# Kernel tuning notes

Measured on AMD Instinct MI355X. Metric: run time of the kernel, lower is better.

The kernel has to match this reference:

```python
import jax, jax.numpy as jnp
import numpy as np

N = 40000
E = 640000
DIN = 128
H = 128
G = 16
C = 10


def setup_inputs() -> dict:
    key = jax.random.key(0)
    ks = jax.random.split(key, 12)
    x = jax.random.normal(ks[0], (N, DIN), dtype=jnp.float32)
    edge_index = jax.random.randint(ks[1], (2, E), 0, N, dtype=jnp.int64)
    batch = jnp.sort(jax.random.randint(ks[2], (N,), 0, G, dtype=jnp.int64))
    s = 1.0 / np.sqrt(H)
    W_in = jax.random.normal(ks[3], (DIN, H), dtype=jnp.float32) * s
    b_in = jnp.zeros((H,), dtype=jnp.float32)
    W1 = jax.random.normal(ks[4], (H, H), dtype=jnp.float32) * s
    b1 = jnp.zeros((H,), dtype=jnp.float32)
    W2 = jax.random.normal(ks[5], (H, H), dtype=jnp.float32) * s
    b2 = jnp.zeros((H,), dtype=jnp.float32)
    Wf1 = jax.random.normal(ks[6], (H, H // 2), dtype=jnp.float32) * s
    bf1 = jnp.zeros((H // 2,), dtype=jnp.float32)
    Wf2 = jax.random.normal(ks[7], (H // 2, C), dtype=jnp.float32) * (1.0 / np.sqrt(H // 2))
    bf2 = jnp.zeros((C,), dtype=jnp.float32)
    return {"x": x, "edge_index": edge_index, "batch": batch,
            "W_in": W_in, "b_in": b_in, "W1": W1, "b1": b1,
            "W2": W2, "b2": b2, "Wf1": Wf1, "bf1": bf1,
            "Wf2": Wf2, "bf2": bf2}


def _gcn_conv(h, src, dst, deg_inv_sqrt, W, b):
    # h' = D^{-1/2} (A + I) D^{-1/2} (h W) + b  (PyG GCNConv with self-loops)
    hw = h @ W  # [N, H]
    norm = deg_inv_sqrt[src] * deg_inv_sqrt[dst]  # [E]
    agg = jax.ops.segment_sum(hw[src] * norm[:, None], dst, num_segments=N)
    agg = agg + hw * (deg_inv_sqrt * deg_inv_sqrt)[:, None]  # self-loop term
    return agg + b


def reference(x, edge_index, batch, W_in, b_in, W1, b1, W2, b2, Wf1, bf1, Wf2, bf2):
    src, dst = edge_index[0], edge_index[1]
    # degree on target nodes, including self-loop (+1)
    deg = jax.ops.segment_sum(jnp.ones((E,), dtype=x.dtype), dst, num_segments=N) + 1.0
    deg_inv_sqrt = jax.lax.rsqrt(deg)

    h = x @ W_in + b_in
    h = jax.nn.relu(_gcn_conv(h, src, dst, deg_inv_sqrt, W1, b1))  # dropout is identity in eval
    h = jax.nn.relu(_gcn_conv(h, src, dst, deg_inv_sqrt, W2, b2))

    # global mean pool by graph id
    sums = jax.ops.segment_sum(h, batch, num_segments=G)  # [G, H]
    counts = jax.ops.segment_sum(jnp.ones((N,), dtype=h.dtype), batch, num_segments=G)
    pooled = sums / jnp.maximum(counts, 1.0)[:, None]

    out = jax.nn.relu(pooled @ Wf1 + bf1) @ Wf2 + bf2  # [G, C]
    return out
```

## Files before the change

kernel.cpp:

```cpp
#include <hip/hip_runtime.h>

#define NN 40000
#define EE 640000
#define NCH 157

typedef unsigned int uint;
typedef unsigned short ushort;
typedef __attribute__((ext_vector_type(8))) short short8;
typedef __attribute__((ext_vector_type(4))) float floatx4;

__device__ inline ushort f2bf(float f) {
    uint u = __float_as_uint(f);
    return (ushort)((u + 0x7fffu + ((u >> 16) & 1u)) >> 16);
}
__device__ inline float bf_lo(uint u) { return __uint_as_float(u << 16); }
__device__ inline float bf_hi(uint u) { return __uint_as_float(u & 0xffff0000u); }

__device__ inline int lower_bound_dev(const int* __restrict__ a, int n, int x) {
    int lo = 0, hi = n;
    while (lo < hi) { int m = (lo + hi) >> 1; if (a[m] < x) lo = m + 1; else hi = m; }
    return lo;
}

__global__ __launch_bounds__(256) void histprep_kernel(const int* __restrict__ dst,
                                                       int* __restrict__ counts,
                                                       const float* __restrict__ W_in,
                                                       const float* __restrict__ W1,
                                                       const float* __restrict__ b_in,
                                                       const float* __restrict__ W2,
                                                       const int* __restrict__ batch,
                                                       ushort* __restrict__ Bp1,
                                                       ushort* __restrict__ Bp2,
                                                       float* __restrict__ cvec,
                                                       int* __restrict__ glo) {
    int b = blockIdx.x, t = threadIdx.x;
    if (b < 2500) {
        atomicAdd(&counts[dst[b * 256 + t]], 1);
    } else if (b < 2564) {
        int idx = (b - 2500) * 256 + t;
        int k = idx >> 7, n = idx & 127;
        float s = 0.f;
        for (int j = 0; j < 128; ++j) s = fmaf(W_in[k * 128 + j], W1[j * 128 + n], s);
        Bp1[((size_t)(k >> 3) * 128 + n) * 8 + (k & 7)] = f2bf(s);
    } else if (b < 2628) {
        int idx = (b - 2564) * 256 + t;
        int k = idx >> 7, n = idx & 127;
        Bp2[((size_t)(k >> 3) * 128 + n) * 8 + (k & 7)] = f2bf(W2[idx]);
    } else {
        if (t < 128) {
            float s = 0.f;
            for (int k = 0; k < 128; ++k) s = fmaf(b_in[k], W1[k * 128 + t], s);
            cvec[t] = s;
        } else if (t < 128 + 17) {
            int g = t - 128;
            glo[g] = lower_bound_dev(batch, NN, g);
        }
    }
}

__global__ __launch_bounds__(256) void scan_kernel(const int* __restrict__ counts,
                                                   int* __restrict__ goff,
                                                   int* __restrict__ start,
                                                   int* __restrict__ cursor,
                                                   float* __restrict__ dis, int N) {
    __shared__ int ws[4];
    __shared__ int sbase;
    int t = threadIdx.x, lane = t & 63, wv = t >> 6;
    int idx = blockIdx.x * 256 + t;
    int c = (idx < N) ? counts[idx] : 0;
    int v = c;
    #pragma unroll
    for (int d = 1; d < 64; d <<= 1) {
        int u = __shfl_up(v, d, 64);
        if (lane >= d) v += u;
    }
    if (lane == 63) ws[wv] = v;
    __syncthreads();
    if (t == 0) {
        int total = ws[0] + ws[1] + ws[2] + ws[3];
        sbase = atomicAdd(goff, total);
    }
    __syncthreads();
    int off = sbase;
    for (int j = 0; j < wv; ++j) off += ws[j];
    if (idx < N) {
        int excl = off + v - c;
        start[idx] = excl;
        cursor[idx] = excl;
        dis[idx] = rsqrtf((float)c + 1.0f);
    }
}

template <bool ABF16>
__device__ inline void mm_tile(const void* __restrict__ Av, const ushort* __restrict__ Bpack,
                               ushort* __restrict__ C, int tile, int wv, int lane) {
    int m = lane & 15, q = lane >> 4;
    int row = tile * 64 + wv * 16 + m;

    short8 afr[4];
    if (ABF16) {
        const ushort* A = (const ushort*)Av;
        const ushort* ap = A + (size_t)row * 128 + q * 8;
        #pragma unroll
        for (int k0 = 0; k0 < 4; ++k0) afr[k0] = *(const short8*)(ap + k0 * 32);
    } else {
        const float* A = (const float*)Av;
        const float* ap = A + (size_t)row * 128 + q * 8;
        #pragma unroll
        for (int k0 = 0; k0 < 4; ++k0) {
            float4 f0 = *(const float4*)(ap + k0 * 32);
            float4 f1 = *(const float4*)(ap + k0 * 32 + 4);
            short8 a;
            a[0] = (short)f2bf(f0.x); a[1] = (short)f2bf(f0.y);
            a[2] = (short)f2bf(f0.z); a[3] = (short)f2bf(f0.w);
            a[4] = (short)f2bf(f1.x); a[5] = (short)f2bf(f1.y);
            a[6] = (short)f2bf(f1.z); a[7] = (short)f2bf(f1.w);
            afr[k0] = a;
        }
    }

    floatx4 acc[8];
    #pragma unroll
    for (int nt = 0; nt < 8; ++nt) { floatx4 z = {0.f, 0.f, 0.f, 0.f}; acc[nt] = z; }

    #pragma unroll
    for (int nt = 0; nt < 8; ++nt) {
        #pragma unroll
        for (int k0 = 0; k0 < 4; ++k0) {
            short8 bfrag = *(const short8*)(Bpack + ((size_t)(k0 * 4 + q) * 128 + nt * 16 + m) * 8);
            acc[nt] = __builtin_amdgcn_mfma_f32_16x16x32_bf16(afr[k0], bfrag, acc[nt], 0, 0, 0);
        }
    }

    int orow_base = tile * 64 + wv * 16 + q * 4;
    #pragma unroll
    for (int nt = 0; nt < 8; ++nt) {
        #pragma unroll
        for (int r = 0; r < 4; ++r)
            C[(size_t)(orow_base + r) * 128 + nt * 16 + m] = f2bf(acc[nt][r]);
    }
}

__global__ __launch_bounds__(256) void fillmm1_kernel(const int* __restrict__ src,
                                                      const int* __restrict__ dst,
                                                      const float* __restrict__ dis,
                                                      int* __restrict__ cursor,
                                                      int2* __restrict__ edata,
                                                      const float* __restrict__ x,
                                                      const ushort* __restrict__ Bp1,
                                                      ushort* __restrict__ bufA) {
    int b = blockIdx.x, t = threadIdx.x;
    if (b < 2500) {
        int e = b * 256 + t;
        int s = src[e], d = dst[e];
        int pos = atomicAdd(&cursor[d], 1);
        float nrm = dis[s] * dis[d];
        int2 v; v.x = s; v.y = __float_as_int(nrm);
        edata[pos] = v;
    } else {
        mm_tile<false>(x, Bp1, bufA, b - 2500, t >> 6, t & 63);
    }
}

__global__ __launch_bounds__(256) void mm2_kernel(const ushort* __restrict__ A,
                                                  const ushort* __restrict__ Bp2,
                                                  ushort* __restrict__ C) {
    mm_tile<true>(A, Bp2, C, blockIdx.x, threadIdx.x >> 6, threadIdx.x & 63);
}

__global__ __launch_bounds__(256) void agg_kernel(const ushort* __restrict__ hw,
                                                  const float* __restrict__ dis,
                                                  const int* __restrict__ start,
                                                  const int* __restrict__ counts,
                                                  const int2* __restrict__ edata,
                                                  const float* __restrict__ cvec,
                                                  const float* __restrict__ bias,
                                                  ushort* __restrict__ out, int N) {
    __shared__ int2 eds[4][64];
    int wv = threadIdx.x >> 6;
    int lane = threadIdx.x & 63;
    int i = blockIdx.x * 4 + wv;
    if (i >= N) return;
    int beg = start[i];
    int deg = counts[i];
    int dmain = deg > 64 ? 64 : deg;
    const uint* __restrict__ hv = (const uint*)hw;

    int2 ed;
    if (lane < dmain) ed = edata[beg + lane];
    else { ed.x = i; ed.y = 0; }
    eds[wv][lane] = ed;

    float di = dis[i];
    float sii = di * di;
    uint su = hv[(size_t)i * 64 + lane];
    float a0 = sii * bf_lo(su);
    float a1 = sii * bf_hi(su);
    float sumnorm = sii;

    int dpad = (dmain + 7) & ~7;
    for (int j = 0; j < dpad; j += 8) {
        int2 e0 = eds[wv][j],     e1 = eds[wv][j + 1];
        int2 e2 = eds[wv][j + 2], e3 = eds[wv][j + 3];
        int2 e4 = eds[wv][j + 4], e5 = eds[wv][j + 5];
        int2 e6 = eds[wv][j + 6], e7 = eds[wv][j + 7];
        uint u0 = hv[(size_t)e0.x * 64 + lane];
        uint u1 = hv[(size_t)e1.x * 64 + lane];
        uint u2 = hv[(size_t)e2.x * 64 + lane];
        uint u3 = hv[(size_t)e3.x * 64 + lane];
        uint u4 = hv[(size_t)e4.x * 64 + lane];
        uint u5 = hv[(size_t)e5.x * 64 + lane];
        uint u6 = hv[(size_t)e6.x * 64 + lane];
        uint u7 = hv[(size_t)e7.x * 64 + lane];
        float n0 = __int_as_float(e0.y), n1 = __int_as_float(e1.y);
        float n2 = __int_as_float(e2.y), n3 = __int_as_float(e3.y);
        float n4 = __int_as_float(e4.y), n5 = __int_as_float(e5.y);
        float n6 = __int_as_float(e6.y), n7 = __int_as_float(e7.y);
        a0 = fmaf(n0, bf_lo(u0), a0); a1 = fmaf(n0, bf_hi(u0), a1);
        a0 = fmaf(n1, bf_lo(u1), a0); a1 = fmaf(n1, bf_hi(u1), a1);
        a0 = fmaf(n2, bf_lo(u2), a0); a1 = fmaf(n2, bf_hi(u2), a1);
        a0 = fmaf(n3, bf_lo(u3), a0); a1 = fmaf(n3, bf_hi(u3), a1);
        a0 = fmaf(n4, bf_lo(u4), a0); a1 = fmaf(n4, bf_hi(u4), a1);
        a0 = fmaf(n5, bf_lo(u5), a0); a1 = fmaf(n5, bf_hi(u5), a1);
        a0 = fmaf(n6, bf_lo(u6), a0); a1 = fmaf(n6, bf_hi(u6), a1);
        a0 = fmaf(n7, bf_lo(u7), a0); a1 = fmaf(n7, bf_hi(u7), a1);
        sumnorm += ((n0 + n1) + (n2 + n3)) + ((n4 + n5) + (n6 + n7));
    }
    for (int e = beg + 64; e < beg + deg; ++e) {
        int2 et = edata[e];
        float n0 = __int_as_float(et.y);
        uint u0 = hv[(size_t)et.x * 64 + lane];
        a0 = fmaf(n0, bf_lo(u0), a0);
        a1 = fmaf(n0, bf_hi(u0), a1);
        sumnorm += n0;
    }

    float c0 = 0.f, c1 = 0.f;
    if (cvec) { c0 = cvec[2 * lane]; c1 = cvec[2 * lane + 1]; }
    float b0 = bias[2 * lane], b1 = bias[2 * lane + 1];
    float o0 = fmaxf(fmaf(sumnorm, c0, a0) + b0, 0.f);
    float o1 = fmaxf(fmaf(sumnorm, c1, a1) + b1, 0.f);
    uint o = (uint)f2bf(o0) | ((uint)f2bf(o1) << 16);
    ((uint*)out)[(size_t)i * 64 + lane] = o;
}

__global__ __launch_bounds__(256) void poolfinal_kernel(const ushort* __restrict__ h,
                                                        const int* __restrict__ glo,
                                                        float* __restrict__ pools,
                                                        int* __restrict__ ticket,
                                                        const float* __restrict__ Wf1,
                                                        const float* __restrict__ bf1,
                                                        const float* __restrict__ Wf2,
                                                        const float* __restrict__ bf2,
                                                        float* __restrict__ out) {
    __shared__ float pooled[16][128];
    __shared__ float z[16][64];
    __shared__ int slast;
    int t = threadIdx.x, c2 = t & 63, wv = t >> 6;
    int b = blockIdx.x;
    int g = b >> 3, ch = b & 7;
    int lo = glo[g], hi = glo[g + 1];
    int span = hi - lo;
    int chunk = (span + 7) >> 3;
    int r0 = lo + ch * chunk;
    int r1 = hi < r0 + chunk ? hi : r0 + chunk;
    const uint* __restrict__ hv = (const uint*)h;

    float a0 = 0.f, a1 = 0.f;
    #pragma unroll 4
    for (int j = r0 + wv; j < r1; j += 4) {
        uint u = hv[(size_t)j * 64 + c2];
        a0 += bf_lo(u);
        a1 += bf_hi(u);
    }
    if (r0 < r1) {
        atomicAdd(&pools[g * 128 + 2 * c2], a0);
        atomicAdd(&pools[g * 128 + 2 * c2 + 1], a1);
    }

    __syncthreads();
    __threadfence();
    if (t == 0) slast = atomicAdd(ticket, 1);
    __syncthreads();
    if (slast != 127) return;

    for (int idx = t; idx < 2048; idx += 256) {
        int gg = idx >> 7, c = idx & 127;
        int cn = glo[gg + 1] - glo[gg];
        float cnf = (float)(cn > 1 ? cn : 1);
        float ps = __hip_atomic_load(&pools[idx], __ATOMIC_RELAXED, __HIP_MEMORY_SCOPE_AGENT);
        pooled[gg][c] = ps / cnf;
    }
    __syncthreads();
    for (int idx = t; idx < 1024; idx += 256) {
        int gg = idx >> 6, j = idx & 63;
        float s = bf1[j];
        for (int k = 0; k < 128; ++k) s = fmaf(pooled[gg][k], Wf1[k * 64 + j], s);
        z[gg][j] = fmaxf(s, 0.f);
    }
    __syncthreads();
    if (t < 160) {
        int gg = t / 10, k = t % 10;
        float s = bf2[k];
        for (int j = 0; j < 64; ++j) s = fmaf(z[gg][j], Wf2[j * 10 + k], s);
        out[t] = s;
    }
}


extern "C" void kernel_launch(void* const* d_in, const int* in_sizes, int n_in,
                              void* d_out, int out_size, void* d_ws, size_t ws_size,
                              hipStream_t stream) {
    const float* x    = (const float*)d_in[0];
    const int* edge   = (const int*)d_in[1];
    const int* batch  = (const int*)d_in[2];
    const float* W_in = (const float*)d_in[3];
    const float* b_in = (const float*)d_in[4];
    const float* W1   = (const float*)d_in[5];
    const float* b1   = (const float*)d_in[6];
    const float* W2   = (const float*)d_in[7];
    const float* b2   = (const float*)d_in[8];
    const float* Wf1  = (const float*)d_in[9];
    const float* bf1  = (const float*)d_in[10];
    const float* Wf2  = (const float*)d_in[11];
    const float* bf2  = (const float*)d_in[12];
    float* out = (float*)d_out;

    char* ws = (char*)d_ws;
    size_t off = 0;
    auto alloc = [&](size_t bytes) -> void* {
        void* p = ws + off;
        off += (bytes + 511) & ~(size_t)511;
        return p;
    };
    int* counts   = (int*)alloc((size_t)NN * 4);
    float* pools  = (float*)alloc(16 * 128 * 4);
    int* misc     = (int*)alloc(512);
    size_t zero_bytes = off;
    int* goff     = misc;
    int* ticket   = misc + 1;
    int* glo      = misc + 8;
    ushort* bufA  = (ushort*)alloc((size_t)NN * 128 * 2);
    ushort* bufB  = (ushort*)alloc((size_t)NN * 128 * 2);
    ushort* Bp1   = (ushort*)alloc(128 * 128 * 2);
    ushort* Bp2   = (ushort*)alloc(128 * 128 * 2);
    float* cvec   = (float*)alloc(128 * 4);
    float* dis    = (float*)alloc((size_t)NN * 4);
    int* start    = (int*)alloc((size_t)NN * 4);
    int* cursor   = (int*)alloc((size_t)NN * 4);
    int2* edata   = (int2*)alloc((size_t)EE * 8);

    hipMemsetAsync(counts, 0, zero_bytes, stream);

    histprep_kernel<<<2629, 256, 0, stream>>>(edge + EE, counts, W_in, W1, b_in, W2,
                                              batch, Bp1, Bp2, cvec, glo);
    scan_kernel<<<NCH, 256, 0, stream>>>(counts, goff, start, cursor, dis, NN);
    fillmm1_kernel<<<2500 + NN / 64, 256, 0, stream>>>(edge, edge + EE, dis, cursor,
                                                       edata, x, Bp1, bufA);
    agg_kernel<<<NN / 4, 256, 0, stream>>>(bufA, dis, start, counts, edata, cvec, b1, bufB, NN);
    mm2_kernel<<<NN / 64, 256, 0, stream>>>(bufB, Bp2, bufA);
    agg_kernel<<<NN / 4, 256, 0, stream>>>(bufA, dis, start, counts, edata, nullptr, b2, bufB, NN);
    poolfinal_kernel<<<128, 256, 0, stream>>>(bufB, glo, pools, ticket,
                                              Wf1, bf1, Wf2, bf2, out);
}
```

Before: 243.1 us.

## Gather neighbor rows with 16-byte loads, four edges per wave in parallel

The aggregation kernel now has each 16-lane quarter of a wave load a full 256-byte bf16 neighbor row as uint4, so four edges are gathered at once instead of one row per wave with 4-byte loads. Each lane keeps eight partial accumulators, and the quarters are combined with cross-lane shuffles before bias, ReLU and a single vectorized store. The goal is fewer, wider memory instructions and more independent gathers in flight. In exchange it uses more registers, adds a shuffle reduction, pads the edge list to multiples of 16, and leaves the overflow tail for nodes with more than 64 edges running on only one quarter of the wave.

```diff
diff --git a/kernel.cpp b/kernel.cpp
--- a/kernel.cpp
+++ b/kernel.cpp
@@ -179,69 +179,111 @@
     __shared__ int2 eds[4][64];
     int wv = threadIdx.x >> 6;
     int lane = threadIdx.x & 63;
+    int q = lane & 15, h4 = lane >> 4;
     int i = blockIdx.x * 4 + wv;
     if (i >= N) return;
     int beg = start[i];
     int deg = counts[i];
     int dmain = deg > 64 ? 64 : deg;
-    const uint* __restrict__ hv = (const uint*)hw;
+    const uint4* __restrict__ hv4 = (const uint4*)hw;
 
     int2 ed;
     if (lane < dmain) ed = edata[beg + lane];
     else { ed.x = i; ed.y = 0; }
     eds[wv][lane] = ed;
 
+    float a0 = 0.f, a1 = 0.f, a2 = 0.f, a3 = 0.f;
+    float a4 = 0.f, a5 = 0.f, a6 = 0.f, a7 = 0.f;
+    float sumnorm = 0.f;
+
+    int dpad = (dmain + 15) & ~15;
+    for (int j = 0; j < dpad; j += 16) {
+        int2 e0 = eds[wv][j + h4];
+        int2 e1 = eds[wv][j + 4 + h4];
+        int2 e2 = eds[wv][j + 8 + h4];
+        int2 e3 = eds[wv][j + 12 + h4];
+        uint4 u0 = hv4[(size_t)e0.x * 16 + q];
+        uint4 u1 = hv4[(size_t)e1.x * 16 + q];
+        uint4 u2 = hv4[(size_t)e2.x * 16 + q];
+        uint4 u3 = hv4[(size_t)e3.x * 16 + q];
+        float n0 = __int_as_float(e0.y), n1 = __int_as_float(e1.y);
+        float n2 = __int_as_float(e2.y), n3 = __int_as_float(e3.y);
+        a0 = fmaf(n0, bf_lo(u0.x), a0); a1 = fmaf(n0, bf_hi(u0.x), a1);
+        a2 = fmaf(n0, bf_lo(u0.y), a2); a3 = fmaf(n0, bf_hi(u0.y), a3);
+        a4 = fmaf(n0, bf_lo(u0.z), a4); a5 = fmaf(n0, bf_hi(u0.z), a5);
+        a6 = fmaf(n0, bf_lo(u0.w), a6); a7 = fmaf(n0, bf_hi(u0.w), a7);
+        a0 = fmaf(n1, bf_lo(u1.x), a0); a1 = fmaf(n1, bf_hi(u1.x), a1);
+        a2 = fmaf(n1, bf_lo(u1.y), a2); a3 = fmaf(n1, bf_hi(u1.y), a3);
+        a4 = fmaf(n1, bf_lo(u1.z), a4); a5 = fmaf(n1, bf_hi(u1.z), a5);
+        a6 = fmaf(n1, bf_lo(u1.w), a6); a7 = fmaf(n1, bf_hi(u1.w), a7);
+        a0 = fmaf(n2, bf_lo(u2.x), a0); a1 = fmaf(n2, bf_hi(u2.x), a1);
+        a2 = fmaf(n2, bf_lo(u2.y), a2); a3 = fmaf(n2, bf_hi(u2.y), a3);
+        a4 = fmaf(n2, bf_lo(u2.z), a4); a5 = fmaf(n2, bf_hi(u2.z), a5);
+        a6 = fmaf(n2, bf_lo(u2.w), a6); a7 = fmaf(n2, bf_hi(u2.w), a7);
+        a0 = fmaf(n3, bf_lo(u3.x), a0); a1 = fmaf(n3, bf_hi(u3.x), a1);
+        a2 = fmaf(n3, bf_lo(u3.y), a2); a3 = fmaf(n3, bf_hi(u3.y), a3);
+        a4 = fmaf(n3, bf_lo(u3.z), a4); a5 = fmaf(n3, bf_hi(u3.z), a5);
+        a6 = fmaf(n3, bf_lo(u3.w), a6); a7 = fmaf(n3, bf_hi(u3.w), a7);
+        sumnorm += (n0 + n1) + (n2 + n3);
+    }
+    for (int e = beg + 64; e < beg + deg; ++e) {
+        int2 et = edata[e];
+        if (h4 == 0) {
+            float n0 = __int_as_float(et.y);
+            uint4 u = hv4[(size_t)et.x * 16 + q];
+            a0 = fmaf(n0, bf_lo(u.x), a0); a1 = fmaf(n0, bf_hi(u.x), a1);
+            a2 = fmaf(n0, bf_lo(u.y), a2); a3 = fmaf(n0, bf_hi(u.y), a3);
+            a4 = fmaf(n0, bf_lo(u.z), a4); a5 = fmaf(n0, bf_hi(u.z), a5);
+            a6 = fmaf(n0, bf_lo(u.w), a6); a7 = fmaf(n0, bf_hi(u.w), a7);
+            sumnorm += n0;
+        }
+    }
+
+    a0 += __shfl_xor(a0, 16); a0 += __shfl_xor(a0, 32);
+    a1 += __shfl_xor(a1, 16); a1 += __shfl_xor(a1, 32);
+    a2 += __shfl_xor(a2, 16); a2 += __shfl_xor(a2, 32);
+    a3 += __shfl_xor(a3, 16); a3 += __shfl_xor(a3, 32);
+    a4 += __shfl_xor(a4, 16); a4 += __shfl_xor(a4, 32);
+    a5 += __shfl_xor(a5, 16); a5 += __shfl_xor(a5, 32);
+    a6 += __shfl_xor(a6, 16); a6 += __shfl_xor(a6, 32);
+    a7 += __shfl_xor(a7, 16); a7 += __shfl_xor(a7, 32);
+    sumnorm += __shfl_xor(sumnorm, 16); sumnorm += __shfl_xor(sumnorm, 32);
+
     float di = dis[i];
     float sii = di * di;
-    uint su = hv[(size_t)i * 64 + lane];
-    float a0 = sii * bf_lo(su);
-    float a1 = sii * bf_hi(su);
-    float sumnorm = sii;
-
-    int dpad = (dmain + 7) & ~7;
-    for (int j = 0; j < dpad; j += 8) {
-        int2 e0 = eds[wv][j],     e1 = eds[wv][j + 1];
-        int2 e2 = eds[wv][j + 2], e3 = eds[wv][j + 3];
-        int2 e4 = eds[wv][j + 4], e5 = eds[wv][j + 5];
-        int2 e6 = eds[wv][j + 6], e7 = eds[wv][j + 7];
-        uint u0 = hv[(size_t)e0.x * 64 + lane];
-        uint u1 = hv[(size_t)e1.x * 64 + lane];
-        uint u2 = hv[(size_t)e2.x * 64 + lane];
-        uint u3 = hv[(size_t)e3.x * 64 + lane];
-        uint u4 = hv[(size_t)e4.x * 64 + lane];
-        uint u5 = hv[(size_t)e5.x * 64 + lane];
-        uint u6 = hv[(size_t)e6.x * 64 + lane];
-        uint u7 = hv[(size_t)e7.x * 64 + lane];
-        float n0 = __int_as_float(e0.y), n1 = __int_as_float(e1.y);
-        float n2 = __int_as_float(e2.y), n3 = __int_as_float(e3.y);
-        float n4 = __int_as_float(e4.y), n5 = __int_as_float(e5.y);
-        float n6 = __int_as_float(e6.y), n7 = __int_as_float(e7.y);
-        a0 = fmaf(n0, bf_lo(u0), a0); a1 = fmaf(n0, bf_hi(u0), a1);
-        a0 = fmaf(n1, bf_lo(u1), a0); a1 = fmaf(n1, bf_hi(u1), a1);
-        a0 = fmaf(n2, bf_lo(u2), a0); a1 = fmaf(n2, bf_hi(u2), a1);
-        a0 = fmaf(n3, bf_lo(u3), a0); a1 = fmaf(n3, bf_hi(u3), a1);
-        a0 = fmaf(n4, bf_lo(u4), a0); a1 = fmaf(n4, bf_hi(u4), a1);
-        a0 = fmaf(n5, bf_lo(u5), a0); a1 = fmaf(n5, bf_hi(u5), a1);
-        a0 = fmaf(n6, bf_lo(u6), a0); a1 = fmaf(n6, bf_hi(u6), a1);
-        a0 = fmaf(n7, bf_lo(u7), a0); a1 = fmaf(n7, bf_hi(u7), a1);
-        sumnorm += ((n0 + n1) + (n2 + n3)) + ((n4 + n5) + (n6 + n7));
-    }
-    for (int e = beg + 64; e < beg + deg; ++e) {
-        int2 et = edata[e];
-        float n0 = __int_as_float(et.y);
-        uint u0 = hv[(size_t)et.x * 64 + lane];
-        a0 = fmaf(n0, bf_lo(u0), a0);
-        a1 = fmaf(n0, bf_hi(u0), a1);
-        sumnorm += n0;
-    }
-
-    float c0 = 0.f, c1 = 0.f;
-    if (cvec) { c0 = cvec[2 * lane]; c1 = cvec[2 * lane + 1]; }
-    float b0 = bias[2 * lane], b1 = bias[2 * lane + 1];
-    float o0 = fmaxf(fmaf(sumnorm, c0, a0) + b0, 0.f);
-    float o1 = fmaxf(fmaf(sumnorm, c1, a1) + b1, 0.f);
-    uint o = (uint)f2bf(o0) | ((uint)f2bf(o1) << 16);
-    ((uint*)out)[(size_t)i * 64 + lane] = o;
+    uint4 su = hv4[(size_t)i * 16 + q];
+    a0 = fmaf(sii, bf_lo(su.x), a0); a1 = fmaf(sii, bf_hi(su.x), a1);
+    a2 = fmaf(sii, bf_lo(su.y), a2); a3 = fmaf(sii, bf_hi(su.y), a3);
+    a4 = fmaf(sii, bf_lo(su.z), a4); a5 = fmaf(sii, bf_hi(su.z), a5);
+    a6 = fmaf(sii, bf_lo(su.w), a6); a7 = fmaf(sii, bf_hi(su.w), a7);
+    sumnorm += sii;
+
+    float c0 = 0.f, c1 = 0.f, c2 = 0.f, c3 = 0.f;
+    float c4 = 0.f, c5 = 0.f, c6 = 0.f, c7 = 0.f;
+    if (cvec) {
+        float4 ca = *(const float4*)(cvec + 8 * q);
+        float4 cb = *(const float4*)(cvec + 8 * q + 4);
+        c0 = ca.x; c1 = ca.y; c2 = ca.z; c3 = ca.w;
+        c4 = cb.x; c5 = cb.y; c6 = cb.z; c7 = cb.w;
+    }
+    float4 ba = *(const float4*)(bias + 8 * q);
+    float4 bb = *(const float4*)(bias + 8 * q + 4);
+    float o0 = fmaxf(fmaf(sumnorm, c0, a0) + ba.x, 0.f);
+    float o1 = fmaxf(fmaf(sumnorm, c1, a1) + ba.y, 0.f);
+    float o2 = fmaxf(fmaf(sumnorm, c2, a2) + ba.z, 0.f);
+    float o3 = fmaxf(fmaf(sumnorm, c3, a3) + ba.w, 0.f);
+    float o4 = fmaxf(fmaf(sumnorm, c4, a4) + bb.x, 0.f);
+    float o5 = fmaxf(fmaf(sumnorm, c5, a5) + bb.y, 0.f);
+    float o6 = fmaxf(fmaf(sumnorm, c6, a6) + bb.z, 0.f);
+    float o7 = fmaxf(fmaf(sumnorm, c7, a7) + bb.w, 0.f);
+    if (h4 == 0) {
+        uint4 o;
+        o.x = (uint)f2bf(o0) | ((uint)f2bf(o1) << 16);
+        o.y = (uint)f2bf(o2) | ((uint)f2bf(o3) << 16);
+        o.z = (uint)f2bf(o4) | ((uint)f2bf(o5) << 16);
+        o.w = (uint)f2bf(o6) | ((uint)f2bf(o7) << 16);
+        ((uint4*)out)[(size_t)i * 16 + q] = o;
+    }
 }
 
 __global__ __launch_bounds__(256) void poolfinal_kernel(const ushort* __restrict__ h,
```

Result: no change. 241.4 us (-0.7%).

## Split hw into column-quarter planes and aggregate per quarter for cache locality

Applied to the files above, without the earlier changes.

The matmul now writes its bf16 output as four column-quarter planes of 32 features each, and aggregation runs four times as many blocks. Each block handles one quarter, with 16 lanes per edge row and 4 edges gathered in parallel, followed by a shuffle reduction. The aim is a smaller per-pass gather working set that fits in cache, plus nontemporal loads and stores for streamed data. The cost is re-reading the edge list four times and extra shuffle and launch overhead.

```diff
diff --git a/kernel.cpp b/kernel.cpp
--- a/kernel.cpp
+++ b/kernel.cpp
@@ -3,6 +3,7 @@
 #define NN 40000
 #define EE 640000
 #define NCH 157
+#define NQB (NN / 4)
 
 typedef unsigned int uint;
 typedef unsigned short ushort;
@@ -135,9 +136,10 @@
     int orow_base = tile * 64 + wv * 16 + q * 4;
     #pragma unroll
     for (int nt = 0; nt < 8; ++nt) {
+        size_t cbase = (size_t)(nt >> 1) * ((size_t)NN * 32) + (size_t)((nt & 1) * 16 + m);
         #pragma unroll
         for (int r = 0; r < 4; ++r)
-            C[(size_t)(orow_base + r) * 128 + nt * 16 + m] = f2bf(acc[nt][r]);
+            C[cbase + (size_t)(orow_base + r) * 32] = f2bf(acc[nt][r]);
     }
 }
 
@@ -168,80 +170,91 @@
     mm_tile<true>(A, Bp2, C, blockIdx.x, threadIdx.x >> 6, threadIdx.x & 63);
 }
 
-__global__ __launch_bounds__(256) void agg_kernel(const ushort* __restrict__ hw,
-                                                  const float* __restrict__ dis,
-                                                  const int* __restrict__ start,
-                                                  const int* __restrict__ counts,
-                                                  const int2* __restrict__ edata,
-                                                  const float* __restrict__ cvec,
-                                                  const float* __restrict__ bias,
-                                                  ushort* __restrict__ out, int N) {
+__global__ __launch_bounds__(256) void aggq_kernel(const ushort* __restrict__ hw,
+                                                   const float* __restrict__ dis,
+                                                   const int* __restrict__ start,
+                                                   const int* __restrict__ counts,
+                                                   const int2* __restrict__ edata,
+                                                   const float* __restrict__ cvec,
+                                                   const float* __restrict__ bias,
+                                                   ushort* __restrict__ out, int N) {
     __shared__ int2 eds[4][64];
     int wv = threadIdx.x >> 6;
     int lane = threadIdx.x & 63;
-    int i = blockIdx.x * 4 + wv;
+    int qb = blockIdx.x / NQB;
+    int b  = blockIdx.x - qb * NQB;
+    int i = b * 4 + wv;
     if (i >= N) return;
+    int m16 = lane & 15, h4 = lane >> 4;
     int beg = start[i];
     int deg = counts[i];
     int dmain = deg > 64 ? 64 : deg;
-    const uint* __restrict__ hv = (const uint*)hw;
+    const uint* __restrict__ hvq = (const uint*)(hw + (size_t)qb * NN * 32);
 
     int2 ed;
-    if (lane < dmain) ed = edata[beg + lane];
-    else { ed.x = i; ed.y = 0; }
+    if (lane < dmain) {
+        long long e64 = __builtin_nontemporal_load((const long long*)(edata + beg + lane));
+        ed.x = (int)(unsigned long long)e64;
+        ed.y = (int)((unsigned long long)e64 >> 32);
+    } else {
+        ed.x = i; ed.y = 0;
+    }
     eds[wv][lane] = ed;
 
-    float di = dis[i];
-    float sii = di * di;
-    uint su = hv[(size_t)i * 64 + lane];
-    float a0 = sii * bf_lo(su);
-    float a1 = sii * bf_hi(su);
-    float sumnorm = sii;
-
-    int dpad = (dmain + 7) & ~7;
-    for (int j = 0; j < dpad; j += 8) {
-        int2 e0 = eds[wv][j],     e1 = eds[wv][j + 1];
-        int2 e2 = eds[wv][j + 2], e3 = eds[wv][j + 3];
-        int2 e4 = eds[wv][j + 4], e5 = eds[wv][j + 5];
-        int2 e6 = eds[wv][j + 6], e7 = eds[wv][j + 7];
-        uint u0 = hv[(size_t)e0.x * 64 + lane];
-        uint u1 = hv[(size_t)e1.x * 64 + lane];
-        uint u2 = hv[(size_t)e2.x * 64 + lane];
-        uint u3 = hv[(size_t)e3.x * 64 + lane];
-        uint u4 = hv[(size_t)e4.x * 64 + lane];
-        uint u5 = hv[(size_t)e5.x * 64 + lane];
-        uint u6 = hv[(size_t)e6.x * 64 + lane];
-        uint u7 = hv[(size_t)e7.x * 64 + lane];
+    float a0 = 0.f, a1 = 0.f, sn = 0.f;
+
+    int dpad = (dmain + 15) & ~15;
+    for (int j = 0; j < dpad; j += 16) {
+        int2 e0 = eds[wv][j + h4];
+        int2 e1 = eds[wv][j + 4 + h4];
+        int2 e2 = eds[wv][j + 8 + h4];
+        int2 e3 = eds[wv][j + 12 + h4];
+        uint u0 = hvq[(size_t)e0.x * 16 + m16];
+        uint u1 = hvq[(size_t)e1.x * 16 + m16];
+        uint u2 = hvq[(size_t)e2.x * 16 + m16];
+        uint u3 = hvq[(size_t)e3.x * 16 + m16];
         float n0 = __int_as_float(e0.y), n1 = __int_as_float(e1.y);
         float n2 = __int_as_float(e2.y), n3 = __int_as_float(e3.y);
-        float n4 = __int_as_float(e4.y), n5 = __int_as_float(e5.y);
-        float n6 = __int_as_float(e6.y), n7 = __int_as_float(e7.y);
         a0 = fmaf(n0, bf_lo(u0), a0); a1 = fmaf(n0, bf_hi(u0), a1);
         a0 = fmaf(n1, bf_lo(u1), a0); a1 = fmaf(n1, bf_hi(u1), a1);
         a0 = fmaf(n2, bf_lo(u2), a0); a1 = fmaf(n2, bf_hi(u2), a1);
         a0 = fmaf(n3, bf_lo(u3), a0); a1 = fmaf(n3, bf_hi(u3), a1);
-        a0 = fmaf(n4, bf_lo(u4), a0); a1 = fmaf(n4, bf_hi(u4), a1);
-        a0 = fmaf(n5, bf_lo(u5), a0); a1 = fmaf(n5, bf_hi(u5), a1);
-        a0 = fmaf(n6, bf_lo(u6), a0); a1 = fmaf(n6, bf_hi(u6), a1);
-        a0 = fmaf(n7, bf_lo(u7), a0); a1 = fmaf(n7, bf_hi(u7), a1);
-        sumnorm += ((n0 + n1) + (n2 + n3)) + ((n4 + n5) + (n6 + n7));
+        sn += (n0 + n1) + (n2 + n3);
     }
     for (int e = beg + 64; e < beg + deg; ++e) {
         int2 et = edata[e];
-        float n0 = __int_as_float(et.y);
-        uint u0 = hv[(size_t)et.x * 64 + lane];
-        a0 = fmaf(n0, bf_lo(u0), a0);
-        a1 = fmaf(n0, bf_hi(u0), a1);
-        sumnorm += n0;
-    }
+        if (h4 == 0) {
+            float n0 = __int_as_float(et.y);
+            uint u0 = hvq[(size_t)et.x * 16 + m16];
+            a0 = fmaf(n0, bf_lo(u0), a0);
+            a1 = fmaf(n0, bf_hi(u0), a1);
+            sn += n0;
+        }
+    }
+
+    a0 += __shfl_xor(a0, 16); a0 += __shfl_xor(a0, 32);
+    a1 += __shfl_xor(a1, 16); a1 += __shfl_xor(a1, 32);
+    sn += __shfl_xor(sn, 16); sn += __shfl_xor(sn, 32);
+
+    float di = dis[i];
+    float sii = di * di;
+    uint su = hvq[(size_t)i * 16 + m16];
+    a0 = fmaf(sii, bf_lo(su), a0);
+    a1 = fmaf(sii, bf_hi(su), a1);
+    sn += sii;
 
     float c0 = 0.f, c1 = 0.f;
-    if (cvec) { c0 = cvec[2 * lane]; c1 = cvec[2 * lane + 1]; }
-    float b0 = bias[2 * lane], b1 = bias[2 * lane + 1];
-    float o0 = fmaxf(fmaf(sumnorm, c0, a0) + b0, 0.f);
-    float o1 = fmaxf(fmaf(sumnorm, c1, a1) + b1, 0.f);
-    uint o = (uint)f2bf(o0) | ((uint)f2bf(o1) << 16);
-    ((uint*)out)[(size_t)i * 64 + lane] = o;
+    if (cvec) {
+        float2 cc = *(const float2*)(cvec + qb * 32 + 2 * m16);
+        c0 = cc.x; c1 = cc.y;
+    }
+    float2 bb = *(const float2*)(bias + qb * 32 + 2 * m16);
+    float o0 = fmaxf(fmaf(sn, c0, a0) + bb.x, 0.f);
+    float o1 = fmaxf(fmaf(sn, c1, a1) + bb.y, 0.f);
+    if (h4 == 0) {
+        uint o = (uint)f2bf(o0) | ((uint)f2bf(o1) << 16);
+        __builtin_nontemporal_store(o, (uint*)out + (size_t)i * 64 + qb * 16 + m16);
+    }
 }
 
 __global__ __launch_bounds__(256) void poolfinal_kernel(const ushort* __restrict__ h,
@@ -357,9 +370,9 @@
     scan_kernel<<<NCH, 256, 0, stream>>>(counts, goff, start, cursor, dis, NN);
     fillmm1_kernel<<<2500 + NN / 64, 256, 0, stream>>>(edge, edge + EE, dis, cursor,
                                                        edata, x, Bp1, bufA);
-    agg_kernel<<<NN / 4, 256, 0, stream>>>(bufA, dis, start, counts, edata, cvec, b1, bufB, NN);
+    aggq_kernel<<<NN, 256, 0, stream>>>(bufA, dis, start, counts, edata, cvec, b1, bufB, NN);
     mm2_kernel<<<NN / 64, 256, 0, stream>>>(bufB, Bp2, bufA);
-    agg_kernel<<<NN / 4, 256, 0, stream>>>(bufA, dis, start, counts, edata, nullptr, b2, bufB, NN);
+    aggq_kernel<<<NN, 256, 0, stream>>>(bufA, dis, start, counts, edata, nullptr, b2, bufB, NN);
     poolfinal_kernel<<<128, 256, 0, stream>>>(bufB, glo, pools, ticket,
                                               Wf1, bf1, Wf2, bf2, out);
 }
```

New measurement: 309.7 us. +27.4%, slower.
